# Kernel tuning notes

Hardware: AMD Instinct MI355X
Metric: run time of the kernel (lower is better)

The kernel has to match this reference:

```python
import jax, jax.numpy as jnp
import numpy as np

N_NODES = 100000
N_EDGES = 1600000
NODE_DIM = 64
EDGE_DIM = 16
HIDDEN_DIM = 64


def setup_inputs() -> dict:
    key = jax.random.key(0)
    ks = jax.random.split(key, 9)
    x = jax.random.normal(ks[0], (N_NODES, NODE_DIM), dtype=jnp.float32)
    edge_index = jax.random.randint(ks[1], (2, N_EDGES), 0, N_NODES, dtype=jnp.int32)
    edge_attr = jax.random.normal(ks[2], (N_EDGES, EDGE_DIM), dtype=jnp.float32)
    msg_in = 2 * NODE_DIM + EDGE_DIM
    s1 = 1.0 / np.sqrt(msg_in)
    s2 = 1.0 / np.sqrt(HIDDEN_DIM)
    su = 1.0 / np.sqrt(NODE_DIM + HIDDEN_DIM)
    W1 = jax.random.uniform(ks[3], (msg_in, HIDDEN_DIM), jnp.float32, -s1, s1)
    b1 = jax.random.uniform(ks[4], (HIDDEN_DIM,), jnp.float32, -s1, s1)
    W2 = jax.random.uniform(ks[5], (HIDDEN_DIM, HIDDEN_DIM), jnp.float32, -s2, s2)
    b2 = jax.random.uniform(ks[6], (HIDDEN_DIM,), jnp.float32, -s2, s2)
    Wu = jax.random.uniform(ks[7], (NODE_DIM + HIDDEN_DIM, NODE_DIM), jnp.float32, -su, su)
    bu = jax.random.uniform(ks[8], (NODE_DIM,), jnp.float32, -su, su)
    return {"x": x, "edge_index": edge_index, "edge_attr": edge_attr,
            "W1": W1, "b1": b1, "W2": W2, "b2": b2, "Wu": Wu, "bu": bu}


def reference(x, edge_index, edge_attr, W1, b1, W2, b2, Wu, bu):
    src, dst = edge_index[0], edge_index[1]
    n_nodes = x.shape[0]
    # gather endpoint features + edge features -> (E, 2*node_dim+edge_dim)
    edge_input = jnp.concatenate([x[src], x[dst], edge_attr], axis=1)
    # message MLP (dropout is identity in eval mode)
    h = jax.nn.relu(edge_input @ W1 + b1)
    messages = h @ W2 + b2  # (E, hidden)
    # scatter-add to dst, count-normalize (mean aggregation)
    aggregated = jax.ops.segment_sum(messages, dst, num_segments=n_nodes)
    counts = jax.ops.segment_sum(jnp.ones((messages.shape[0], 1), x.dtype), dst,
                                 num_segments=n_nodes)
    aggregated = aggregated / (counts + 1e-6)
    # update MLP + residual
    update_input = jnp.concatenate([x, aggregated], axis=1)
    x_new = jax.nn.relu(update_input @ Wu + bu)
    return x + x_new
```

## Files before the change

### kernel.cpp

```cpp
#include <hip/hip_runtime.h>

#define N_NODES  100000
#define N_EDGES  1600000
#define NODE_DIM 64
#define EDGE_DIM 16
#define HIDDEN   64
#define N_GROUPS 100000
#define EDGE_BLOCKS 768

typedef __bf16 bf16x8 __attribute__((ext_vector_type(8)));
typedef unsigned short u16x8 __attribute__((ext_vector_type(8)));
typedef unsigned short u16x4 __attribute__((ext_vector_type(4)));
typedef float f32x4 __attribute__((ext_vector_type(4)));
typedef float f32x2 __attribute__((ext_vector_type(2)));

__device__ __forceinline__ unsigned short f2bf(float f) {
    unsigned int u = __float_as_uint(f);
    u += 0x7FFFu + ((u >> 16) & 1u);
    return (unsigned short)(u >> 16);
}

__device__ __forceinline__ float bf2f(unsigned short s) {
    return __uint_as_float((unsigned int)s << 16);
}

__device__ __forceinline__ bf16x8 lds_frag(const unsigned short* p) {
    return __builtin_bit_cast(bf16x8, *(const u16x8*)p);
}

__device__ __forceinline__ void cvt16v(unsigned short* dst,
                                       float4 f0, float4 f1, float4 f2, float4 f3) {
    u16x8 p0, p1;
    p0[0]=f2bf(f0.x); p0[1]=f2bf(f0.y); p0[2]=f2bf(f0.z); p0[3]=f2bf(f0.w);
    p0[4]=f2bf(f1.x); p0[5]=f2bf(f1.y); p0[6]=f2bf(f1.z); p0[7]=f2bf(f1.w);
    p1[0]=f2bf(f2.x); p1[1]=f2bf(f2.y); p1[2]=f2bf(f2.z); p1[3]=f2bf(f2.w);
    p1[4]=f2bf(f3.x); p1[5]=f2bf(f3.y); p1[6]=f2bf(f3.z); p1[7]=f2bf(f3.w);
    *(u16x8*)dst       = p0;
    *(u16x8*)(dst + 8) = p1;
}

__device__ __forceinline__ void cvt4v(unsigned short* dst, float4 f) {
    u16x4 p;
    p[0]=f2bf(f.x); p[1]=f2bf(f.y); p[2]=f2bf(f.z); p[3]=f2bf(f.w);
    *(u16x4*)dst = p;
}

__device__ __forceinline__ void atomic_pk_add_bf16(unsigned short* p, unsigned int v) {
    asm volatile("global_atomic_pk_add_bf16 %0, %1, off"
                 :: "v"(p), "v"(v) : "memory");
}

__global__ void prep_kernel(const float* __restrict__ W1, const float* __restrict__ W2,
                            const float* __restrict__ Wu, const float* __restrict__ x,
                            unsigned short* __restrict__ W1t,
                            unsigned short* __restrict__ W2t,
                            unsigned short* __restrict__ Wut,
                            unsigned short* __restrict__ xb)
{
    int t = blockIdx.x * 256 + threadIdx.x;
    int stride = gridDim.x * 256;
    for (int i = t; i < N_NODES * 64 / 4; i += stride) {
        float4 f = ((const float4*)x)[i];
        cvt4v(&xb[i * 4], f);
    }
    for (int i = t; i < 64 * 160; i += stride) {
        int n = i / 160, k = i % 160;
        W1t[i] = (k < 144) ? f2bf(W1[k * 64 + n]) : (unsigned short)0;
    }
    for (int i = t; i < 64 * 64; i += stride) {
        int n = i / 64, k = i % 64;
        W2t[i] = f2bf(W2[k * 64 + n]);
    }
    for (int i = t; i < 64 * 128; i += stride) {
        int n = i / 128, k = i % 128;
        Wut[i] = f2bf(Wu[k * 64 + n]);
    }
}

#define SA  168
#define SW1 164
#define SH  72
#define WAVE_LDS (16*SA*2 + 16*SH*2)

__global__ __launch_bounds__(256, 3) void edge_kernel(
    const unsigned short* __restrict__ xb,
    const int*   __restrict__ ei,
    const float* __restrict__ ea,
    const unsigned short* __restrict__ W1t,
    const unsigned short* __restrict__ W2t,
    const float* __restrict__ b1,
    const float* __restrict__ b2,
    unsigned short* __restrict__ agg,
    float* __restrict__ cnt)
{
    __shared__ __align__(16) unsigned short sW1[64 * SW1];
    __shared__ __align__(16) unsigned char  sAH[4 * WAVE_LDS];
    __shared__ int sdst[64];

    const int t    = threadIdx.x;
    const int lane = t & 63;
    const int w    = t >> 6;

    #pragma unroll
    for (int i = 0; i < 5; i++) {
        int c = t + i * 256;
        int n = c / 20, k8 = c % 20;
        *(u16x8*)&sW1[n * SW1 + k8 * 8] = *(const u16x8*)&W1t[c * 8];
    }
    __syncthreads();

    unsigned short* myAin = (unsigned short*)(sAH + w * WAVE_LDS);
    float*          myMsg = (float*)myAin;
    unsigned short* myH   = (unsigned short*)(sAH + w * WAVE_LDS + 16 * SA * 2);

    if (lane < 16) {
        u16x8 z = {0,0,0,0,0,0,0,0};
        *(u16x8*)&myAin[lane * SA + 144] = z;
        *(u16x8*)&myAin[lane * SA + 152] = z;
    }

    const int col = lane & 15;
    const int kq  = lane >> 4;
    const int el  = lane >> 2;
    const int q   = lane & 3;
    const int c2  = lane & 31;
    const int eh  = lane >> 5;

    float b1r[4], b2r[4];
    u16x8 w2f[8];
    #pragma unroll
    for (int ct = 0; ct < 4; ct++) {
        b1r[ct] = b1[ct * 16 + col];
        b2r[ct] = b2[ct * 16 + col];
        #pragma unroll
        for (int ks = 0; ks < 2; ks++)
            w2f[ks * 4 + ct] = *(const u16x8*)&W2t[(ct * 16 + col) * 64 + ks * 32 + kq * 8];
    }

    const int TW = EDGE_BLOCKS * 4;
    const int gw = blockIdx.x * 4 + w;

    int d_cur;
    u16x8 gx[4];
    float4 fe;
    {
        int e = gw * 16 + el;
        int s = ei[e];
        d_cur = ei[N_EDGES + e];
        const u16x8* ps = (const u16x8*)(xb + (size_t)s * 64);
        const u16x8* pd = (const u16x8*)(xb + (size_t)d_cur * 64);
        gx[0] = ps[2 * q]; gx[1] = ps[2 * q + 1];
        gx[2] = pd[2 * q]; gx[3] = pd[2 * q + 1];
        fe = ((const float4*)ea)[(size_t)gw * 64 + lane];
    }

    for (int g = gw; g < N_GROUPS; g += TW) {
        const int gn = g + TW;
        const bool more = gn < N_GROUPS;
        int sn = 0, dn = 0;
        if (more) {
            int e2 = gn * 16 + el;
            sn = ei[e2];
            dn = ei[N_EDGES + e2];
        }

        unsigned short* row = myAin + el * SA;
        *(u16x8*)(row + q * 16)          = gx[0];
        *(u16x8*)(row + q * 16 + 8)      = gx[1];
        *(u16x8*)(row + 64 + q * 16)     = gx[2];
        *(u16x8*)(row + 64 + q * 16 + 8) = gx[3];
        cvt4v(&row[128 + q * 4], fe);
        if (q == 1) sdst[w * 16 + el] = d_cur;
        if (q == 2) atomicAdd(&cnt[d_cur], 1.0f);

        if (more) {
            const u16x8* ps = (const u16x8*)(xb + (size_t)sn * 64);
            const u16x8* pd = (const u16x8*)(xb + (size_t)dn * 64);
            gx[0] = ps[2 * q]; gx[1] = ps[2 * q + 1];
            gx[2] = pd[2 * q]; gx[3] = pd[2 * q + 1];
            fe = ((const float4*)ea)[(size_t)gn * 64 + lane];
        }
        d_cur = dn;

        __builtin_amdgcn_wave_barrier();

        f32x4 acc[4] = {{0,0,0,0},{0,0,0,0},{0,0,0,0},{0,0,0,0}};
        #pragma unroll
        for (int ks = 0; ks < 5; ks++) {
            int ko = ks * 32 + kq * 8;
            bf16x8 a = lds_frag(&myAin[col * SA + ko]);
            #pragma unroll
            for (int ct = 0; ct < 4; ct++) {
                bf16x8 b = lds_frag(&sW1[(ct * 16 + col) * SW1 + ko]);
                acc[ct] = __builtin_amdgcn_mfma_f32_16x16x32_bf16(a, b, acc[ct], 0, 0, 0);
            }
        }
        #pragma unroll
        for (int ct = 0; ct < 4; ct++) {
            #pragma unroll
            for (int r = 0; r < 4; r++)
                myH[(kq * 4 + r) * SH + ct * 16 + col] =
                    f2bf(fmaxf(acc[ct][r] + b1r[ct], 0.0f));
        }
        __builtin_amdgcn_wave_barrier();

        f32x4 m[4] = {{0,0,0,0},{0,0,0,0},{0,0,0,0},{0,0,0,0}};
        #pragma unroll
        for (int ks = 0; ks < 2; ks++) {
            int ko = ks * 32 + kq * 8;
            bf16x8 a = lds_frag(&myH[col * SH + ko]);
            #pragma unroll
            for (int ct = 0; ct < 4; ct++)
                m[ct] = __builtin_amdgcn_mfma_f32_16x16x32_bf16(
                    a, __builtin_bit_cast(bf16x8, w2f[ks * 4 + ct]), m[ct], 0, 0, 0);
        }
        #pragma unroll
        for (int ct = 0; ct < 4; ct++) {
            #pragma unroll
            for (int r = 0; r < 4; r++)
                myMsg[(kq * 4 + r) * 84 + ct * 16 + col] = m[ct][r] + b2r[ct];
        }
        __builtin_amdgcn_wave_barrier();

        #pragma unroll 1
        for (int i = 0; i < 8; i++) {
            int   el2 = i * 2 + eh;
            int   dd  = sdst[w * 16 + el2];
            f32x2 v   = *(const f32x2*)&myMsg[el2 * 84 + c2 * 2];
            unsigned int pk = ((unsigned int)f2bf(v[1]) << 16) | f2bf(v[0]);
            atomic_pk_add_bf16(&agg[(size_t)dd * 64 + c2 * 2], pk);
        }
        __builtin_amdgcn_wave_barrier();
    }
}

#define NSA 136
__global__ __launch_bounds__(256, 4) void node_kernel(
    const float* __restrict__ x,
    const unsigned short* __restrict__ agg,
    const float* __restrict__ cnt,
    const unsigned short* __restrict__ Wut,
    const float* __restrict__ bu,
    float* __restrict__ out)
{
    __shared__ __align__(16) unsigned short sA [64 * NSA];
    __shared__ __align__(16) unsigned short sWu[64 * NSA];
    const int t = threadIdx.x, lane = t & 63, w = t >> 6;
    const int n0 = blockIdx.x * 64;

    #pragma unroll
    for (int i = 0; i < 4; i++) {
        int c = t + i * 256;
        int n = c / 16, k8 = c % 16;
        *(u16x8*)&sWu[n * NSA + k8 * 8] = *(const u16x8*)&Wut[c * 8];
    }
    {
        const int nl = t >> 2, q = t & 3;
        const int n = n0 + nl;
        unsigned short* row = sA + nl * NSA;
        if (n < N_NODES) {
            const float4* px = (const float4*)(x + (size_t)n * 64);
            cvt16v(row + q * 16, px[q*4], px[q*4+1], px[q*4+2], px[q*4+3]);
            float inv = 1.0f / (cnt[n] + 1e-6f);
            const u16x8* pa = (const u16x8*)(agg + (size_t)n * 64);
            u16x8 a0 = pa[2 * q], a1 = pa[2 * q + 1];
            u16x8 r0, r1;
            #pragma unroll
            for (int j = 0; j < 8; j++) {
                r0[j] = f2bf(bf2f(a0[j]) * inv);
                r1[j] = f2bf(bf2f(a1[j]) * inv);
            }
            *(u16x8*)(row + 64 + q * 16)     = r0;
            *(u16x8*)(row + 64 + q * 16 + 8) = r1;
        } else {
            u16x8 z = {0,0,0,0,0,0,0,0};
            *(u16x8*)&row[q * 16]          = z;
            *(u16x8*)&row[q * 16 + 8]      = z;
            *(u16x8*)&row[64 + q * 16]     = z;
            *(u16x8*)&row[64 + q * 16 + 8] = z;
        }
    }
    __syncthreads();

    const int col = lane & 15, kq = lane >> 4;
    const int arow = w * 16 + col;
    f32x4 acc[4] = {{0,0,0,0},{0,0,0,0},{0,0,0,0},{0,0,0,0}};
    #pragma unroll
    for (int ks = 0; ks < 4; ks++) {
        int ko = ks * 32 + kq * 8;
        bf16x8 a = lds_frag(&sA[arow * NSA + ko]);
        #pragma unroll
        for (int ct = 0; ct < 4; ct++) {
            bf16x8 b = lds_frag(&sWu[(ct * 16 + col) * NSA + ko]);
            acc[ct] = __builtin_amdgcn_mfma_f32_16x16x32_bf16(a, b, acc[ct], 0, 0, 0);
        }
    }
    #pragma unroll
    for (int ct = 0; ct < 4; ct++) {
        float bb = bu[ct * 16 + col];
        #pragma unroll
        for (int r = 0; r < 4; r++) {
            int row = w * 16 + kq * 4 + r;
            int n = n0 + row;
            if (n < N_NODES) {
                int c2 = ct * 16 + col;
                float xa = x[(size_t)n * 64 + c2];
                out[(size_t)n * 64 + c2] = xa + fmaxf(acc[ct][r] + bb, 0.0f);
            }
        }
    }
}

extern "C" void kernel_launch(void* const* d_in, const int* in_sizes, int n_in,
                              void* d_out, int out_size, void* d_ws, size_t ws_size,
                              hipStream_t stream) {
    const float* x  = (const float*)d_in[0];
    const int*   ei = (const int*)  d_in[1];
    const float* ea = (const float*)d_in[2];
    const float* W1 = (const float*)d_in[3];
    const float* b1 = (const float*)d_in[4];
    const float* W2 = (const float*)d_in[5];
    const float* b2 = (const float*)d_in[6];
    const float* Wu = (const float*)d_in[7];
    const float* bu = (const float*)d_in[8];
    float* out = (float*)d_out;

    unsigned short* agg = (unsigned short*)d_ws;
    float* cnt = (float*)(agg + (size_t)N_NODES * HIDDEN);
    unsigned short* W1t = (unsigned short*)(cnt + N_NODES);
    unsigned short* W2t = W1t + 64 * 160;
    unsigned short* Wut = W2t + 64 * 64;
    unsigned short* xb  = Wut + 64 * 128;

    hipMemsetAsync(d_ws, 0,
                   (size_t)N_NODES * HIDDEN * sizeof(unsigned short)
                   + (size_t)N_NODES * sizeof(float), stream);

    prep_kernel<<<512, 256, 0, stream>>>(W1, W2, Wu, x, W1t, W2t, Wut, xb);
    edge_kernel<<<EDGE_BLOCKS, 256, 0, stream>>>(xb, ei, ea, W1t, W2t, b1, b2, agg, cnt);
    node_kernel<<<(N_NODES + 63) / 64, 256, 0, stream>>>(x, agg, cnt, Wut, bu, out);
}
```

Baseline: 469.8 us.

## Replace edge-parallel atomic scatter with CSR-sorted node-parallel aggregation

Builds a destination-sorted CSR edge list each call (degree count, three-kernel prefix scan, atomic fill) and computes messages per destination node, reducing them in registers via shuffles. This removes the bf16 packed atomics into the aggregation buffer and the float count atomics, and folds the mean normalization into the aggregation kernel. In exchange it adds several kernels, an extra edge-list buffer, random gathers of edge attributes, and wasted MFMA work on partially filled 16-edge groups.

```diff
diff --git a/kernel.cpp b/kernel.cpp
--- a/kernel.cpp
+++ b/kernel.cpp
@@ -5,14 +5,13 @@
 #define NODE_DIM 64
 #define EDGE_DIM 16
 #define HIDDEN   64
-#define N_GROUPS 100000
-#define EDGE_BLOCKS 768
+#define AGG_BLOCKS 768
+#define NB1 ((N_NODES + 255) / 256)
 
 typedef __bf16 bf16x8 __attribute__((ext_vector_type(8)));
 typedef unsigned short u16x8 __attribute__((ext_vector_type(8)));
 typedef unsigned short u16x4 __attribute__((ext_vector_type(4)));
 typedef float f32x4 __attribute__((ext_vector_type(4)));
-typedef float f32x2 __attribute__((ext_vector_type(2)));
 
 __device__ __forceinline__ unsigned short f2bf(float f) {
     unsigned int u = __float_as_uint(f);
@@ -45,17 +44,14 @@
     *(u16x4*)dst = p;
 }
 
-__device__ __forceinline__ void atomic_pk_add_bf16(unsigned short* p, unsigned int v) {
-    asm volatile("global_atomic_pk_add_bf16 %0, %1, off"
-                 :: "v"(p), "v"(v) : "memory");
-}
-
 __global__ void prep_kernel(const float* __restrict__ W1, const float* __restrict__ W2,
                             const float* __restrict__ Wu, const float* __restrict__ x,
+                            const int* __restrict__ ei,
                             unsigned short* __restrict__ W1t,
                             unsigned short* __restrict__ W2t,
                             unsigned short* __restrict__ Wut,
-                            unsigned short* __restrict__ xb)
+                            unsigned short* __restrict__ xb,
+                            int* __restrict__ deg)
 {
     int t = blockIdx.x * 256 + threadIdx.x;
     int stride = gridDim.x * 256;
@@ -63,6 +59,8 @@
         float4 f = ((const float4*)x)[i];
         cvt4v(&xb[i * 4], f);
     }
+    for (int e = t; e < N_EDGES; e += stride)
+        atomicAdd(&deg[ei[N_EDGES + e]], 1);
     for (int i = t; i < 64 * 160; i += stride) {
         int n = i / 160, k = i % 160;
         W1t[i] = (k < 144) ? f2bf(W1[k * 64 + n]) : (unsigned short)0;
@@ -74,6 +72,60 @@
     for (int i = t; i < 64 * 128; i += stride) {
         int n = i / 128, k = i % 128;
         Wut[i] = f2bf(Wu[k * 64 + n]);
+    }
+}
+
+__global__ void scan1_kernel(const int* __restrict__ deg, int* __restrict__ ofs,
+                             int* __restrict__ bsum) {
+    __shared__ int sh[256];
+    int t = threadIdx.x, i = blockIdx.x * 256 + t;
+    int v = (i < N_NODES) ? deg[i] : 0;
+    sh[t] = v; __syncthreads();
+    #pragma unroll
+    for (int o = 1; o < 256; o <<= 1) {
+        int add = (t >= o) ? sh[t - o] : 0;
+        __syncthreads();
+        sh[t] += add;
+        __syncthreads();
+    }
+    if (i < N_NODES) ofs[i] = sh[t] - v;
+    if (t == 255) bsum[blockIdx.x] = sh[t];
+}
+
+__global__ void scan2_kernel(int* __restrict__ bsum) {
+    __shared__ int sh[512];
+    int t = threadIdx.x;
+    int v = (t < NB1) ? bsum[t] : 0;
+    sh[t] = v; __syncthreads();
+    #pragma unroll
+    for (int o = 1; o < 512; o <<= 1) {
+        int add = (t >= o) ? sh[t - o] : 0;
+        __syncthreads();
+        sh[t] += add;
+        __syncthreads();
+    }
+    if (t < NB1) bsum[t] = sh[t] - v;
+}
+
+__global__ void scan3_kernel(int* __restrict__ ofs, const int* __restrict__ bsum,
+                             int* __restrict__ cur) {
+    int t = threadIdx.x, i = blockIdx.x * 256 + t;
+    if (i < N_NODES) {
+        int o = ofs[i] + bsum[blockIdx.x];
+        ofs[i] = o;
+        cur[i] = o;
+    }
+}
+
+__global__ void fill_kernel(const int* __restrict__ ei, int* __restrict__ cur,
+                            long long* __restrict__ elist) {
+    int idx = blockIdx.x * 256 + threadIdx.x;
+    int stride = gridDim.x * 256;
+    for (int e = idx; e < N_EDGES; e += stride) {
+        int s = ei[e];
+        int d = ei[N_EDGES + e];
+        int pos = atomicAdd(&cur[d], 1);
+        elist[pos] = ((long long)e << 32) | (unsigned int)s;
     }
 }
 
@@ -82,20 +134,20 @@
 #define SH  72
 #define WAVE_LDS (16*SA*2 + 16*SH*2)
 
-__global__ __launch_bounds__(256, 3) void edge_kernel(
+__global__ __launch_bounds__(256, 3) void agg_kernel(
     const unsigned short* __restrict__ xb,
-    const int*   __restrict__ ei,
     const float* __restrict__ ea,
+    const long long* __restrict__ elist,
+    const int* __restrict__ ofs,
+    const int* __restrict__ deg,
     const unsigned short* __restrict__ W1t,
     const unsigned short* __restrict__ W2t,
     const float* __restrict__ b1,
     const float* __restrict__ b2,
-    unsigned short* __restrict__ agg,
-    float* __restrict__ cnt)
+    unsigned short* __restrict__ agg)
 {
     __shared__ __align__(16) unsigned short sW1[64 * SW1];
     __shared__ __align__(16) unsigned char  sAH[4 * WAVE_LDS];
-    __shared__ int sdst[64];
 
     const int t    = threadIdx.x;
     const int lane = t & 63;
@@ -110,7 +162,6 @@
     __syncthreads();
 
     unsigned short* myAin = (unsigned short*)(sAH + w * WAVE_LDS);
-    float*          myMsg = (float*)myAin;
     unsigned short* myH   = (unsigned short*)(sAH + w * WAVE_LDS + 16 * SA * 2);
 
     if (lane < 16) {
@@ -123,8 +174,6 @@
     const int kq  = lane >> 4;
     const int el  = lane >> 2;
     const int q   = lane & 3;
-    const int c2  = lane & 31;
-    const int eh  = lane >> 5;
 
     float b1r[4], b2r[4];
     u16x8 w2f[8];
@@ -137,100 +186,88 @@
             w2f[ks * 4 + ct] = *(const u16x8*)&W2t[(ct * 16 + col) * 64 + ks * 32 + kq * 8];
     }
 
-    const int TW = EDGE_BLOCKS * 4;
-    const int gw = blockIdx.x * 4 + w;
-
-    int d_cur;
-    u16x8 gx[4];
-    float4 fe;
-    {
-        int e = gw * 16 + el;
-        int s = ei[e];
-        d_cur = ei[N_EDGES + e];
-        const u16x8* ps = (const u16x8*)(xb + (size_t)s * 64);
-        const u16x8* pd = (const u16x8*)(xb + (size_t)d_cur * 64);
-        gx[0] = ps[2 * q]; gx[1] = ps[2 * q + 1];
-        gx[2] = pd[2 * q]; gx[3] = pd[2 * q + 1];
-        fe = ((const float4*)ea)[(size_t)gw * 64 + lane];
-    }
-
-    for (int g = gw; g < N_GROUPS; g += TW) {
-        const int gn = g + TW;
-        const bool more = gn < N_GROUPS;
-        int sn = 0, dn = 0;
-        if (more) {
-            int e2 = gn * 16 + el;
-            sn = ei[e2];
-            dn = ei[N_EDGES + e2];
-        }
-
-        unsigned short* row = myAin + el * SA;
-        *(u16x8*)(row + q * 16)          = gx[0];
-        *(u16x8*)(row + q * 16 + 8)      = gx[1];
-        *(u16x8*)(row + 64 + q * 16)     = gx[2];
-        *(u16x8*)(row + 64 + q * 16 + 8) = gx[3];
-        cvt4v(&row[128 + q * 4], fe);
-        if (q == 1) sdst[w * 16 + el] = d_cur;
-        if (q == 2) atomicAdd(&cnt[d_cur], 1.0f);
-
-        if (more) {
-            const u16x8* ps = (const u16x8*)(xb + (size_t)sn * 64);
-            const u16x8* pd = (const u16x8*)(xb + (size_t)dn * 64);
-            gx[0] = ps[2 * q]; gx[1] = ps[2 * q + 1];
-            gx[2] = pd[2 * q]; gx[3] = pd[2 * q + 1];
-            fe = ((const float4*)ea)[(size_t)gn * 64 + lane];
-        }
-        d_cur = dn;
-
-        __builtin_amdgcn_wave_barrier();
-
-        f32x4 acc[4] = {{0,0,0,0},{0,0,0,0},{0,0,0,0},{0,0,0,0}};
-        #pragma unroll
-        for (int ks = 0; ks < 5; ks++) {
-            int ko = ks * 32 + kq * 8;
-            bf16x8 a = lds_frag(&myAin[col * SA + ko]);
+    const int TW = AGG_BLOCKS * 4;
+    for (int n = blockIdx.x * 4 + w; n < N_NODES; n += TW) {
+        const int dg = deg[n];
+        if (dg == 0) {
+            agg[(size_t)n * 64 + lane] = 0;
+            continue;
+        }
+        const int base = ofs[n];
+        const u16x8* pd = (const u16x8*)(xb + (size_t)n * 64);
+        const u16x8 d0 = pd[2 * q], d1 = pd[2 * q + 1];
+
+        float aggv[4] = {0.f, 0.f, 0.f, 0.f};
+
+        for (int g0 = 0; g0 < dg; g0 += 16) {
+            const int rem = (dg - g0 < 16) ? (dg - g0) : 16;
+
+            long long se = 0;
+            if (el < rem) se = elist[base + g0 + el];
+            const int srci = (int)(se & 0xffffffffLL);
+            const int eid  = (int)(se >> 32);
+            const u16x8* ps = (const u16x8*)(xb + (size_t)srci * 64);
+            u16x8 s0 = ps[2 * q], s1 = ps[2 * q + 1];
+            float4 fe = ((const float4*)ea)[(size_t)eid * 4 + q];
+
+            unsigned short* row = myAin + el * SA;
+            *(u16x8*)(row + q * 16)          = s0;
+            *(u16x8*)(row + q * 16 + 8)      = s1;
+            *(u16x8*)(row + 64 + q * 16)     = d0;
+            *(u16x8*)(row + 64 + q * 16 + 8) = d1;
+            cvt4v(&row[128 + q * 4], fe);
+            __builtin_amdgcn_wave_barrier();
+
+            f32x4 acc[4] = {{0,0,0,0},{0,0,0,0},{0,0,0,0},{0,0,0,0}};
+            #pragma unroll
+            for (int ks = 0; ks < 5; ks++) {
+                int ko = ks * 32 + kq * 8;
+                bf16x8 a = lds_frag(&myAin[col * SA + ko]);
+                #pragma unroll
+                for (int ct = 0; ct < 4; ct++) {
+                    bf16x8 b = lds_frag(&sW1[(ct * 16 + col) * SW1 + ko]);
+                    acc[ct] = __builtin_amdgcn_mfma_f32_16x16x32_bf16(a, b, acc[ct], 0, 0, 0);
+                }
+            }
             #pragma unroll
             for (int ct = 0; ct < 4; ct++) {
-                bf16x8 b = lds_frag(&sW1[(ct * 16 + col) * SW1 + ko]);
-                acc[ct] = __builtin_amdgcn_mfma_f32_16x16x32_bf16(a, b, acc[ct], 0, 0, 0);
-            }
-        }
-        #pragma unroll
-        for (int ct = 0; ct < 4; ct++) {
+                #pragma unroll
+                for (int r = 0; r < 4; r++)
+                    myH[(kq * 4 + r) * SH + ct * 16 + col] =
+                        f2bf(fmaxf(acc[ct][r] + b1r[ct], 0.0f));
+            }
+            __builtin_amdgcn_wave_barrier();
+
+            f32x4 m[4] = {{0,0,0,0},{0,0,0,0},{0,0,0,0},{0,0,0,0}};
             #pragma unroll
-            for (int r = 0; r < 4; r++)
-                myH[(kq * 4 + r) * SH + ct * 16 + col] =
-                    f2bf(fmaxf(acc[ct][r] + b1r[ct], 0.0f));
-        }
-        __builtin_amdgcn_wave_barrier();
-
-        f32x4 m[4] = {{0,0,0,0},{0,0,0,0},{0,0,0,0},{0,0,0,0}};
-        #pragma unroll
-        for (int ks = 0; ks < 2; ks++) {
-            int ko = ks * 32 + kq * 8;
-            bf16x8 a = lds_frag(&myH[col * SH + ko]);
+            for (int ks = 0; ks < 2; ks++) {
+                int ko = ks * 32 + kq * 8;
+                bf16x8 a = lds_frag(&myH[col * SH + ko]);
+                #pragma unroll
+                for (int ct = 0; ct < 4; ct++)
+                    m[ct] = __builtin_amdgcn_mfma_f32_16x16x32_bf16(
+                        a, __builtin_bit_cast(bf16x8, w2f[ks * 4 + ct]), m[ct], 0, 0, 0);
+            }
+            __builtin_amdgcn_wave_barrier();
+
             #pragma unroll
-            for (int ct = 0; ct < 4; ct++)
-                m[ct] = __builtin_amdgcn_mfma_f32_16x16x32_bf16(
-                    a, __builtin_bit_cast(bf16x8, w2f[ks * 4 + ct]), m[ct], 0, 0, 0);
-        }
-        #pragma unroll
-        for (int ct = 0; ct < 4; ct++) {
-            #pragma unroll
-            for (int r = 0; r < 4; r++)
-                myMsg[(kq * 4 + r) * 84 + ct * 16 + col] = m[ct][r] + b2r[ct];
-        }
-        __builtin_amdgcn_wave_barrier();
-
-        #pragma unroll 1
-        for (int i = 0; i < 8; i++) {
-            int   el2 = i * 2 + eh;
-            int   dd  = sdst[w * 16 + el2];
-            f32x2 v   = *(const f32x2*)&myMsg[el2 * 84 + c2 * 2];
-            unsigned int pk = ((unsigned int)f2bf(v[1]) << 16) | f2bf(v[0]);
-            atomic_pk_add_bf16(&agg[(size_t)dd * 64 + c2 * 2], pk);
-        }
-        __builtin_amdgcn_wave_barrier();
+            for (int ct = 0; ct < 4; ct++) {
+                float ssum = 0.0f;
+                #pragma unroll
+                for (int r = 0; r < 4; r++) {
+                    float v = m[ct][r] + b2r[ct];
+                    ssum += ((kq * 4 + r) < rem) ? v : 0.0f;
+                }
+                ssum += __shfl_xor(ssum, 16);
+                ssum += __shfl_xor(ssum, 32);
+                aggv[ct] += ssum;
+            }
+        }
+
+        const float scale = 1.0f / ((float)dg + 1e-6f);
+        float vout = (kq == 0) ? aggv[0] : (kq == 1) ? aggv[1]
+                   : (kq == 2) ? aggv[2] : aggv[3];
+        agg[(size_t)n * 64 + lane] = f2bf(vout * scale);
     }
 }
 
@@ -238,7 +275,6 @@
 __global__ __launch_bounds__(256, 4) void node_kernel(
     const float* __restrict__ x,
     const unsigned short* __restrict__ agg,
-    const float* __restrict__ cnt,
     const unsigned short* __restrict__ Wut,
     const float* __restrict__ bu,
     float* __restrict__ out)
@@ -261,17 +297,9 @@
         if (n < N_NODES) {
             const float4* px = (const float4*)(x + (size_t)n * 64);
             cvt16v(row + q * 16, px[q*4], px[q*4+1], px[q*4+2], px[q*4+3]);
-            float inv = 1.0f / (cnt[n] + 1e-6f);
             const u16x8* pa = (const u16x8*)(agg + (size_t)n * 64);
-            u16x8 a0 = pa[2 * q], a1 = pa[2 * q + 1];
-            u16x8 r0, r1;
-            #pragma unroll
-            for (int j = 0; j < 8; j++) {
-                r0[j] = f2bf(bf2f(a0[j]) * inv);
-                r1[j] = f2bf(bf2f(a1[j]) * inv);
-            }
-            *(u16x8*)(row + 64 + q * 16)     = r0;
-            *(u16x8*)(row + 64 + q * 16 + 8) = r1;
+            *(u16x8*)(row + 64 + q * 16)     = pa[2 * q];
+            *(u16x8*)(row + 64 + q * 16 + 8) = pa[2 * q + 1];
         } else {
             u16x8 z = {0,0,0,0,0,0,0,0};
             *(u16x8*)&row[q * 16]          = z;
@@ -326,17 +354,24 @@
     float* out = (float*)d_out;
 
     unsigned short* agg = (unsigned short*)d_ws;
-    float* cnt = (float*)(agg + (size_t)N_NODES * HIDDEN);
-    unsigned short* W1t = (unsigned short*)(cnt + N_NODES);
+    int* deg  = (int*)(agg + (size_t)N_NODES * HIDDEN);
+    int* ofs  = deg + N_NODES;
+    int* cur  = ofs + N_NODES;
+    int* bsum = cur + N_NODES;
+    long long* elist = (long long*)(bsum + 512);
+    unsigned short* W1t = (unsigned short*)(elist + N_EDGES);
     unsigned short* W2t = W1t + 64 * 160;
     unsigned short* Wut = W2t + 64 * 64;
     unsigned short* xb  = Wut + 64 * 128;
 
-    hipMemsetAsync(d_ws, 0,
-                   (size_t)N_NODES * HIDDEN * sizeof(unsigned short)
-                   + (size_t)N_NODES * sizeof(float), stream);
-
-    prep_kernel<<<512, 256, 0, stream>>>(W1, W2, Wu, x, W1t, W2t, Wut, xb);
-    edge_kernel<<<EDGE_BLOCKS, 256, 0, stream>>>(xb, ei, ea, W1t, W2t, b1, b2, agg, cnt);
-    node_kernel<<<(N_NODES + 63) / 64, 256, 0, stream>>>(x, agg, cnt, Wut, bu, out);
-}
+    hipMemsetAsync(deg, 0, (size_t)N_NODES * sizeof(int), stream);
+
+    prep_kernel<<<512, 256, 0, stream>>>(W1, W2, Wu, x, ei, W1t, W2t, Wut, xb, deg);
+    scan1_kernel<<<NB1, 256, 0, stream>>>(deg, ofs, bsum);
+    scan2_kernel<<<1, 512, 0, stream>>>(bsum);
+    scan3_kernel<<<NB1, 256, 0, stream>>>(ofs, bsum, cur);
+    fill_kernel<<<1024, 256, 0, stream>>>(ei, cur, elist);
+    agg_kernel<<<AGG_BLOCKS, 256, 0, stream>>>(xb, ea, elist, ofs, deg,
+                                               W1t, W2t, b1, b2, agg);
+    node_kernel<<<(N_NODES + 63) / 64, 256, 0, stream>>>(x, agg, Wut, bu, out);
+}
```

Result: slower. 765.0 us (+62.8%).

## Bucket edges by destination block and fuse aggregation with node update

Applied to the files above, without the earlier changes.

Edges are counting-sorted into buckets of 64 destination nodes using a histogram, a single-block scan and a fill pass that packs src and local-dst into metadata and converts edge attributes to bf16. One fused kernel per bucket runs the message MLP, accumulates messages and degrees in shared-memory fp32 atomics, then applies the update MLP directly. This removes the global bf16 packed atomics, the agg/cnt buffers and the separate node kernel, and improves aggregation precision. The cost is extra passes over edges for histogram and scatter, plus possible load imbalance across buckets.

```diff
diff --git a/kernel.cpp b/kernel.cpp
--- a/kernel.cpp
+++ b/kernel.cpp
@@ -5,14 +5,13 @@
 #define NODE_DIM 64
 #define EDGE_DIM 16
 #define HIDDEN   64
-#define N_GROUPS 100000
-#define EDGE_BLOCKS 768
+#define NBKT     1563
+#define NB1 ((N_NODES + 255) / 256)
 
 typedef __bf16 bf16x8 __attribute__((ext_vector_type(8)));
 typedef unsigned short u16x8 __attribute__((ext_vector_type(8)));
 typedef unsigned short u16x4 __attribute__((ext_vector_type(4)));
 typedef float f32x4 __attribute__((ext_vector_type(4)));
-typedef float f32x2 __attribute__((ext_vector_type(2)));
 
 __device__ __forceinline__ unsigned short f2bf(float f) {
     unsigned int u = __float_as_uint(f);
@@ -45,17 +44,14 @@
     *(u16x4*)dst = p;
 }
 
-__device__ __forceinline__ void atomic_pk_add_bf16(unsigned short* p, unsigned int v) {
-    asm volatile("global_atomic_pk_add_bf16 %0, %1, off"
-                 :: "v"(p), "v"(v) : "memory");
-}
-
 __global__ void prep_kernel(const float* __restrict__ W1, const float* __restrict__ W2,
                             const float* __restrict__ Wu, const float* __restrict__ x,
+                            const int* __restrict__ ei,
                             unsigned short* __restrict__ W1t,
                             unsigned short* __restrict__ W2t,
                             unsigned short* __restrict__ Wut,
-                            unsigned short* __restrict__ xb)
+                            unsigned short* __restrict__ xb,
+                            int* __restrict__ bhist)
 {
     int t = blockIdx.x * 256 + threadIdx.x;
     int stride = gridDim.x * 256;
@@ -63,6 +59,8 @@
         float4 f = ((const float4*)x)[i];
         cvt4v(&xb[i * 4], f);
     }
+    for (int e = t; e < N_EDGES; e += stride)
+        atomicAdd(&bhist[ei[N_EDGES + e] >> 6], 1);
     for (int i = t; i < 64 * 160; i += stride) {
         int n = i / 160, k = i % 160;
         W1t[i] = (k < 144) ? f2bf(W1[k * 64 + n]) : (unsigned short)0;
@@ -77,29 +75,80 @@
     }
 }
 
-#define SA  168
-#define SW1 164
-#define SH  72
+#define SCN 2048
+__global__ void bscan_kernel(const int* __restrict__ bhist,
+                             int* __restrict__ bofs, int* __restrict__ bcur) {
+    __shared__ int s0[SCN], s1[SCN];
+    const int t = threadIdx.x;
+    for (int i = t; i < SCN; i += 1024) s0[i] = (i < NBKT) ? bhist[i] : 0;
+    __syncthreads();
+    int* src = s0; int* dst = s1;
+    for (int off = 1; off < SCN; off <<= 1) {
+        for (int i = t; i < SCN; i += 1024)
+            dst[i] = (i >= off) ? src[i] + src[i - off] : src[i];
+        __syncthreads();
+        int* tmp = src; src = dst; dst = tmp;
+    }
+    for (int i = t; i < NBKT; i += 1024) {
+        int e = (i > 0) ? src[i - 1] : 0;
+        bofs[i] = e; bcur[i] = e;
+    }
+    if (t == 0) bofs[NBKT] = N_EDGES;
+}
+
+__global__ void bfill_kernel(const int* __restrict__ ei, const float* __restrict__ ea,
+                             int* __restrict__ bcur,
+                             unsigned int* __restrict__ meta,
+                             unsigned short* __restrict__ ea_s)
+{
+    int idx = blockIdx.x * 256 + threadIdx.x;
+    int stride = gridDim.x * 256;
+    if (idx < 128) meta[N_EDGES + idx] = 0;
+    if (idx < 256) {
+        u16x8 z = {0,0,0,0,0,0,0,0};
+        ((u16x8*)(ea_s + (size_t)N_EDGES * 16))[idx] = z;
+    }
+    for (int e = idx; e < N_EDGES; e += stride) {
+        int s = ei[e];
+        int d = ei[N_EDGES + e];
+        int pos = atomicAdd(&bcur[d >> 6], 1);
+        meta[pos] = ((unsigned int)(d & 63) << 17) | (unsigned int)s;
+        const float4* pe = (const float4*)(ea + (size_t)e * 16);
+        cvt16v(ea_s + (size_t)pos * 16, pe[0], pe[1], pe[2], pe[3]);
+    }
+}
+
+#define SA   168
+#define SW1  164
+#define SH   72
+#define NSA  136
+#define SACC 65
 #define WAVE_LDS (16*SA*2 + 16*SH*2)
 
-__global__ __launch_bounds__(256, 3) void edge_kernel(
+__global__ __launch_bounds__(256, 2) void bagg_kernel(
     const unsigned short* __restrict__ xb,
-    const int*   __restrict__ ei,
-    const float* __restrict__ ea,
+    const unsigned short* __restrict__ ea_s,
+    const unsigned int*  __restrict__ meta,
+    const int* __restrict__ bofs,
     const unsigned short* __restrict__ W1t,
     const unsigned short* __restrict__ W2t,
     const float* __restrict__ b1,
     const float* __restrict__ b2,
-    unsigned short* __restrict__ agg,
-    float* __restrict__ cnt)
+    const unsigned short* __restrict__ Wut,
+    const float* __restrict__ bu,
+    const float* __restrict__ x,
+    float* __restrict__ out)
 {
     __shared__ __align__(16) unsigned short sW1[64 * SW1];
+    __shared__ __align__(16) float          sAcc[64 * SACC];
     __shared__ __align__(16) unsigned char  sAH[4 * WAVE_LDS];
-    __shared__ int sdst[64];
+    __shared__ int   sdstoff[4 * 16];
+    __shared__ float sdeg[64];
 
     const int t    = threadIdx.x;
     const int lane = t & 63;
     const int w    = t >> 6;
+    const int b    = blockIdx.x;
 
     #pragma unroll
     for (int i = 0; i < 5; i++) {
@@ -107,10 +156,11 @@
         int n = c / 20, k8 = c % 20;
         *(u16x8*)&sW1[n * SW1 + k8 * 8] = *(const u16x8*)&W1t[c * 8];
     }
+    for (int i = t; i < 64 * SACC; i += 256) sAcc[i] = 0.0f;
+    if (t < 64) sdeg[t] = 0.0f;
     __syncthreads();
 
     unsigned short* myAin = (unsigned short*)(sAH + w * WAVE_LDS);
-    float*          myMsg = (float*)myAin;
     unsigned short* myH   = (unsigned short*)(sAH + w * WAVE_LDS + 16 * SA * 2);
 
     if (lane < 16) {
@@ -123,8 +173,6 @@
     const int kq  = lane >> 4;
     const int el  = lane >> 2;
     const int q   = lane & 3;
-    const int c2  = lane & 31;
-    const int eh  = lane >> 5;
 
     float b1r[4], b2r[4];
     u16x8 w2f[8];
@@ -137,52 +185,42 @@
             w2f[ks * 4 + ct] = *(const u16x8*)&W2t[(ct * 16 + col) * 64 + ks * 32 + kq * 8];
     }
 
-    const int TW = EDGE_BLOCKS * 4;
-    const int gw = blockIdx.x * 4 + w;
-
-    int d_cur;
-    u16x8 gx[4];
-    float4 fe;
-    {
-        int e = gw * 16 + el;
-        int s = ei[e];
-        d_cur = ei[N_EDGES + e];
-        const u16x8* ps = (const u16x8*)(xb + (size_t)s * 64);
-        const u16x8* pd = (const u16x8*)(xb + (size_t)d_cur * 64);
-        gx[0] = ps[2 * q]; gx[1] = ps[2 * q + 1];
-        gx[2] = pd[2 * q]; gx[3] = pd[2 * q + 1];
-        fe = ((const float4*)ea)[(size_t)gw * 64 + lane];
-    }
-
-    for (int g = gw; g < N_GROUPS; g += TW) {
-        const int gn = g + TW;
-        const bool more = gn < N_GROUPS;
-        int sn = 0, dn = 0;
-        if (more) {
-            int e2 = gn * 16 + el;
-            sn = ei[e2];
-            dn = ei[N_EDGES + e2];
-        }
-
-        unsigned short* row = myAin + el * SA;
-        *(u16x8*)(row + q * 16)          = gx[0];
-        *(u16x8*)(row + q * 16 + 8)      = gx[1];
-        *(u16x8*)(row + 64 + q * 16)     = gx[2];
-        *(u16x8*)(row + 64 + q * 16 + 8) = gx[3];
-        cvt4v(&row[128 + q * 4], fe);
-        if (q == 1) sdst[w * 16 + el] = d_cur;
-        if (q == 2) atomicAdd(&cnt[d_cur], 1.0f);
-
-        if (more) {
-            const u16x8* ps = (const u16x8*)(xb + (size_t)sn * 64);
-            const u16x8* pd = (const u16x8*)(xb + (size_t)dn * 64);
-            gx[0] = ps[2 * q]; gx[1] = ps[2 * q + 1];
-            gx[2] = pd[2 * q]; gx[3] = pd[2 * q + 1];
-            fe = ((const float4*)ea)[(size_t)gn * 64 + lane];
-        }
-        d_cur = dn;
-
+    const int base = bofs[b];
+    const int ecnt = bofs[b + 1] - base;
+    const int ng   = (ecnt + 15) >> 4;
+
+    unsigned int pk = meta[base + w * 16 + el];
+    int srcc = (int)(pk & 0x1FFFF);
+    int dstc = (int)(pk >> 17);
+    const u16x8* ps = (const u16x8*)(xb + (size_t)srcc * 64);
+    u16x8 gx0 = ps[2 * q], gx1 = ps[2 * q + 1];
+    const u16x8* pd = (const u16x8*)(xb + (size_t)(b * 64 + dstc) * 64);
+    u16x8 dx0 = pd[2 * q], dx1 = pd[2 * q + 1];
+    u16x4 fe = *(const u16x4*)&ea_s[(size_t)(base + w * 16 + el) * 16 + q * 4];
+
+    for (int g = w; g < ng; g += 4) {
+        const int remv = ecnt - g * 16;
+        const int rem  = remv < 16 ? remv : 16;
+
+        unsigned int pkN = meta[base + (g + 4) * 16 + el];
+
+        unsigned short* rowp = myAin + el * SA;
+        *(u16x8*)(rowp + q * 16)          = gx0;
+        *(u16x8*)(rowp + q * 16 + 8)      = gx1;
+        *(u16x8*)(rowp + 64 + q * 16)     = dx0;
+        *(u16x8*)(rowp + 64 + q * 16 + 8) = dx1;
+        *(u16x4*)(rowp + 128 + q * 4)     = fe;
+        if (q == 1) sdstoff[w * 16 + el] = dstc;
+        if (q == 2 && el < rem) atomicAdd(&sdeg[dstc], 1.0f);
         __builtin_amdgcn_wave_barrier();
+
+        int srcN = (int)(pkN & 0x1FFFF);
+        int dstN = (int)(pkN >> 17);
+        const u16x8* psN = (const u16x8*)(xb + (size_t)srcN * 64);
+        u16x8 gxN0 = psN[2 * q], gxN1 = psN[2 * q + 1];
+        const u16x8* pdN = (const u16x8*)(xb + (size_t)(b * 64 + dstN) * 64);
+        u16x8 dxN0 = pdN[2 * q], dxN1 = pdN[2 * q + 1];
+        u16x4 feN = *(const u16x4*)&ea_s[(size_t)(base + (g + 4) * 16 + el) * 16 + q * 4];
 
         f32x4 acc[4] = {{0,0,0,0},{0,0,0,0},{0,0,0,0},{0,0,0,0}};
         #pragma unroll
@@ -191,8 +229,8 @@
             bf16x8 a = lds_frag(&myAin[col * SA + ko]);
             #pragma unroll
             for (int ct = 0; ct < 4; ct++) {
-                bf16x8 b = lds_frag(&sW1[(ct * 16 + col) * SW1 + ko]);
-                acc[ct] = __builtin_amdgcn_mfma_f32_16x16x32_bf16(a, b, acc[ct], 0, 0, 0);
+                bf16x8 bb = lds_frag(&sW1[(ct * 16 + col) * SW1 + ko]);
+                acc[ct] = __builtin_amdgcn_mfma_f32_16x16x32_bf16(a, bb, acc[ct], 0, 0, 0);
             }
         }
         #pragma unroll
@@ -214,85 +252,73 @@
                 m[ct] = __builtin_amdgcn_mfma_f32_16x16x32_bf16(
                     a, __builtin_bit_cast(bf16x8, w2f[ks * 4 + ct]), m[ct], 0, 0, 0);
         }
+        __builtin_amdgcn_wave_barrier();
+
+        int dsto[4];
+        #pragma unroll
+        for (int r = 0; r < 4; r++) dsto[r] = sdstoff[w * 16 + kq * 4 + r];
         #pragma unroll
         for (int ct = 0; ct < 4; ct++) {
             #pragma unroll
-            for (int r = 0; r < 4; r++)
-                myMsg[(kq * 4 + r) * 84 + ct * 16 + col] = m[ct][r] + b2r[ct];
+            for (int r = 0; r < 4; r++) {
+                if (kq * 4 + r < rem)
+                    atomicAdd(&sAcc[dsto[r] * SACC + ct * 16 + col],
+                              m[ct][r] + b2r[ct]);
+            }
         }
         __builtin_amdgcn_wave_barrier();
 
-        #pragma unroll 1
-        for (int i = 0; i < 8; i++) {
-            int   el2 = i * 2 + eh;
-            int   dd  = sdst[w * 16 + el2];
-            f32x2 v   = *(const f32x2*)&myMsg[el2 * 84 + c2 * 2];
-            unsigned int pk = ((unsigned int)f2bf(v[1]) << 16) | f2bf(v[0]);
-            atomic_pk_add_bf16(&agg[(size_t)dd * 64 + c2 * 2], pk);
-        }
-        __builtin_amdgcn_wave_barrier();
-    }
-}
-
-#define NSA 136
-__global__ __launch_bounds__(256, 4) void node_kernel(
-    const float* __restrict__ x,
-    const unsigned short* __restrict__ agg,
-    const float* __restrict__ cnt,
-    const unsigned short* __restrict__ Wut,
-    const float* __restrict__ bu,
-    float* __restrict__ out)
-{
-    __shared__ __align__(16) unsigned short sA [64 * NSA];
-    __shared__ __align__(16) unsigned short sWu[64 * NSA];
-    const int t = threadIdx.x, lane = t & 63, w = t >> 6;
-    const int n0 = blockIdx.x * 64;
+        gx0 = gxN0; gx1 = gxN1; dx0 = dxN0; dx1 = dxN1; fe = feN; dstc = dstN;
+    }
+
+    __syncthreads();
+
+    unsigned short* sWu_n = (unsigned short*)sAH;
+    unsigned short* sA_n  = sW1;
+    const int n0 = b * 64;
 
     #pragma unroll
     for (int i = 0; i < 4; i++) {
         int c = t + i * 256;
         int n = c / 16, k8 = c % 16;
-        *(u16x8*)&sWu[n * NSA + k8 * 8] = *(const u16x8*)&Wut[c * 8];
+        *(u16x8*)&sWu_n[n * NSA + k8 * 8] = *(const u16x8*)&Wut[c * 8];
     }
     {
-        const int nl = t >> 2, q = t & 3;
+        const int nl = t >> 2, qq = t & 3;
         const int n = n0 + nl;
-        unsigned short* row = sA + nl * NSA;
+        unsigned short* row = sA_n + nl * NSA;
         if (n < N_NODES) {
             const float4* px = (const float4*)(x + (size_t)n * 64);
-            cvt16v(row + q * 16, px[q*4], px[q*4+1], px[q*4+2], px[q*4+3]);
-            float inv = 1.0f / (cnt[n] + 1e-6f);
-            const u16x8* pa = (const u16x8*)(agg + (size_t)n * 64);
-            u16x8 a0 = pa[2 * q], a1 = pa[2 * q + 1];
+            cvt16v(row + qq * 16, px[qq*4], px[qq*4+1], px[qq*4+2], px[qq*4+3]);
+            float inv = 1.0f / (sdeg[nl] + 1e-6f);
             u16x8 r0, r1;
             #pragma unroll
             for (int j = 0; j < 8; j++) {
-                r0[j] = f2bf(bf2f(a0[j]) * inv);
-                r1[j] = f2bf(bf2f(a1[j]) * inv);
+                r0[j] = f2bf(sAcc[nl * SACC + qq * 16 + j] * inv);
+                r1[j] = f2bf(sAcc[nl * SACC + qq * 16 + 8 + j] * inv);
             }
-            *(u16x8*)(row + 64 + q * 16)     = r0;
-            *(u16x8*)(row + 64 + q * 16 + 8) = r1;
+            *(u16x8*)(row + 64 + qq * 16)     = r0;
+            *(u16x8*)(row + 64 + qq * 16 + 8) = r1;
         } else {
             u16x8 z = {0,0,0,0,0,0,0,0};
-            *(u16x8*)&row[q * 16]          = z;
-            *(u16x8*)&row[q * 16 + 8]      = z;
-            *(u16x8*)&row[64 + q * 16]     = z;
-            *(u16x8*)&row[64 + q * 16 + 8] = z;
+            *(u16x8*)&row[qq * 16]          = z;
+            *(u16x8*)&row[qq * 16 + 8]      = z;
+            *(u16x8*)&row[64 + qq * 16]     = z;
+            *(u16x8*)&row[64 + qq * 16 + 8] = z;
         }
     }
     __syncthreads();
 
-    const int col = lane & 15, kq = lane >> 4;
     const int arow = w * 16 + col;
     f32x4 acc[4] = {{0,0,0,0},{0,0,0,0},{0,0,0,0},{0,0,0,0}};
     #pragma unroll
     for (int ks = 0; ks < 4; ks++) {
         int ko = ks * 32 + kq * 8;
-        bf16x8 a = lds_frag(&sA[arow * NSA + ko]);
+        bf16x8 a = lds_frag(&sA_n[arow * NSA + ko]);
         #pragma unroll
         for (int ct = 0; ct < 4; ct++) {
-            bf16x8 b = lds_frag(&sWu[(ct * 16 + col) * NSA + ko]);
-            acc[ct] = __builtin_amdgcn_mfma_f32_16x16x32_bf16(a, b, acc[ct], 0, 0, 0);
+            bf16x8 bb = lds_frag(&sWu_n[(ct * 16 + col) * NSA + ko]);
+            acc[ct] = __builtin_amdgcn_mfma_f32_16x16x32_bf16(a, bb, acc[ct], 0, 0, 0);
         }
     }
     #pragma unroll
@@ -325,18 +351,21 @@
     const float* bu = (const float*)d_in[8];
     float* out = (float*)d_out;
 
-    unsigned short* agg = (unsigned short*)d_ws;
-    float* cnt = (float*)(agg + (size_t)N_NODES * HIDDEN);
-    unsigned short* W1t = (unsigned short*)(cnt + N_NODES);
+    unsigned int* meta = (unsigned int*)d_ws;
+    unsigned short* ea_s = (unsigned short*)(meta + N_EDGES + 128);
+    unsigned short* W1t = ea_s + (size_t)(N_EDGES + 128) * 16;
     unsigned short* W2t = W1t + 64 * 160;
     unsigned short* Wut = W2t + 64 * 64;
     unsigned short* xb  = Wut + 64 * 128;
-
-    hipMemsetAsync(d_ws, 0,
-                   (size_t)N_NODES * HIDDEN * sizeof(unsigned short)
-                   + (size_t)N_NODES * sizeof(float), stream);
-
-    prep_kernel<<<512, 256, 0, stream>>>(W1, W2, Wu, x, W1t, W2t, Wut, xb);
-    edge_kernel<<<EDGE_BLOCKS, 256, 0, stream>>>(xb, ei, ea, W1t, W2t, b1, b2, agg, cnt);
-    node_kernel<<<(N_NODES + 63) / 64, 256, 0, stream>>>(x, agg, cnt, Wut, bu, out);
-}
+    int* bhist = (int*)(xb + (size_t)(N_NODES + 64) * 64);
+    int* bofs  = bhist + NBKT;
+    int* bcur  = bofs + NBKT + 1;
+
+    hipMemsetAsync(bhist, 0, NBKT * sizeof(int), stream);
+
+    prep_kernel<<<512, 256, 0, stream>>>(W1, W2, Wu, x, ei, W1t, W2t, Wut, xb, bhist);
+    bscan_kernel<<<1, 1024, 0, stream>>>(bhist, bofs, bcur);
+    bfill_kernel<<<1024, 256, 0, stream>>>(ei, ea, bcur, meta, ea_s);
+    bagg_kernel<<<NBKT, 256, 0, stream>>>(xb, ea_s, meta, bofs,
+                                          W1t, W2t, b1, b2, Wut, bu, x, out);
+}
```

Measured after the change: 1.516 ms. +222.8%, slower.
